# Performance work log

Hardware: AMD Instinct MI355X
Metric: run time of the kernel (lower is better)

Reference implementation:

```python
import jax, jax.numpy as jnp
import numpy as np

INPUT_SIZE = 1
HIDDEN = 30
B, T = 8192, 512


def setup_inputs() -> dict:
    key = jax.random.key(0)
    ks = jax.random.split(key, 7)
    s_ih = 1.0 / np.sqrt(HIDDEN)
    batch = jax.random.normal(ks[0], (B, T, INPUT_SIZE), dtype=jnp.float32)
    # PyTorch LSTM params: gate order i, f, g, o stacked along first dim (4H)
    W_ih = jax.random.uniform(ks[1], (4 * HIDDEN, INPUT_SIZE), minval=-s_ih, maxval=s_ih, dtype=jnp.float32)
    W_hh = jax.random.uniform(ks[2], (4 * HIDDEN, HIDDEN), minval=-s_ih, maxval=s_ih, dtype=jnp.float32)
    b_ih = jax.random.uniform(ks[3], (4 * HIDDEN,), minval=-s_ih, maxval=s_ih, dtype=jnp.float32)
    b_hh = jax.random.uniform(ks[4], (4 * HIDDEN,), minval=-s_ih, maxval=s_ih, dtype=jnp.float32)
    W_fc = jax.random.uniform(ks[5], (1, HIDDEN), minval=-s_ih, maxval=s_ih, dtype=jnp.float32)
    b_fc = jax.random.uniform(ks[6], (1,), minval=-s_ih, maxval=s_ih, dtype=jnp.float32)
    return {"batch": batch, "W_ih": W_ih, "W_hh": W_hh, "b_ih": b_ih, "b_hh": b_hh, "W_fc": W_fc, "b_fc": b_fc}


def _lstm_final_h(x, W_ih, W_hh, b_ih, b_hh):
    # x: [B, T, I] -> final hidden state h_T: [B, H]
    Bx = x.shape[0]
    H = W_hh.shape[1]
    # Precompute input-side gate projections for all timesteps: [T, B, 4H]
    xg = jnp.einsum('bti,gi->tbg', x, W_ih) + (b_ih + b_hh)

    def step(carry, xt):
        h, c = carry
        gates = xt + h @ W_hh.T  # [B, 4H]
        i, f, g, o = jnp.split(gates, 4, axis=-1)
        i = jax.nn.sigmoid(i)
        f = jax.nn.sigmoid(f)
        g = jnp.tanh(g)
        o = jax.nn.sigmoid(o)
        c = f * c + i * g
        h = o * jnp.tanh(c)
        return (h, c), None

    h0 = jnp.zeros((Bx, H), dtype=x.dtype)
    c0 = jnp.zeros((Bx, H), dtype=x.dtype)
    (hT, _), _ = jax.lax.scan(step, (h0, c0), xg)
    return hT


def reference(batch, W_ih, W_hh, b_ih, b_hh, W_fc, b_fc):
    hT = _lstm_final_h(batch, W_ih, W_hh, b_ih, b_hh)  # [B, H]
    out = hT @ W_fc.T + b_fc  # [B, 1]
    return out.squeeze(-1)  # [B]
```

## Files before the change

### kernel.cpp

```cpp
#include <hip/hip_runtime.h>

#define HID 30
#define TS  512
#define NB  16
#define LOG2E 1.44269504088896340736f
#define XSTR 17
#define HS   40

typedef __attribute__((ext_vector_type(8))) short bf16x8;
typedef __attribute__((ext_vector_type(4))) float f32x4;

__device__ __forceinline__ float rcp_f(float x){ return __builtin_amdgcn_rcpf(x); }
__device__ __forceinline__ float ex2_f(float x){ return __builtin_amdgcn_exp2f(x); }

__global__ __launch_bounds__(512, 4)
void lstm_mfma_u1(const float* __restrict__ batch,
                  const float* __restrict__ W_ih,
                  const float* __restrict__ W_hh,
                  const float* __restrict__ b_ih,
                  const float* __restrict__ b_hh,
                  const float* __restrict__ W_fc,
                  const float* __restrict__ b_fc,
                  float* __restrict__ out)
{
    __shared__ int xs[TS * XSTR];
    __shared__ __align__(16) short hhi[2][NB][HS];
    __shared__ __align__(16) short hlo[2][NB][HS];

    const int tid  = threadIdx.x;
    const int w    = tid >> 6;
    const int lane = tid & 63;
    const int q    = lane >> 4;
    const int col  = lane & 15;
    const int b0   = blockIdx.x * NB;

    #pragma unroll 4
    for (int i = 0; i < NB; ++i) {
        const float v = batch[(size_t)(b0 + i) * TS + tid];
        const __bf16 xh = (__bf16)v;
        const __bf16 xl = (__bf16)(v - (float)xh);
        xs[tid * XSTR + i] =
            (int)((unsigned)__builtin_bit_cast(unsigned short, xh) |
                 ((unsigned)__builtin_bit_cast(unsigned short, xl) << 16));
    }
    for (int i = tid; i < 2 * NB * HS / 2; i += 512) {
        ((int*)hhi)[i] = 0;
        ((int*)hlo)[i] = 0;
    }

    bf16x8 ahi, alo;
    {
        const int gate = col & 3;
        const int unit = 4 * w + (col >> 2);
        const float sG = (gate == 2) ? (-2.0f * LOG2E) : (-LOG2E);
        const int R = gate * HID + unit;
        #pragma unroll
        for (int jj = 0; jj < 8; ++jj) {
            const int kk = q * 8 + jj;
            float wv = 0.0f;
            if (unit < HID) {
                if (kk < HID)      wv = W_hh[R * HID + kk];
                else if (kk == 30) wv = b_ih[R] + b_hh[R];
                else               wv = W_ih[R];
            }
            wv *= sG;
            const __bf16 hi = (__bf16)wv;
            const __bf16 lo = (__bf16)(wv - (float)hi);
            ahi[jj] = (short)__builtin_bit_cast(unsigned short, hi);
            alo[jj] = (short)__builtin_bit_cast(unsigned short, lo);
        }
    }

    __syncthreads();

    const float TWOL = 2.0f * LOG2E;
    float cm = 0.0f;

#define STEP(T, RB, WB)                                                        \
{                                                                              \
    int4 vhi = *(const int4*)&hhi[RB][col][8 * q];                             \
    int4 vlo = *(const int4*)&hlo[RB][col][8 * q];                             \
    const unsigned xp = (unsigned)xs[(T) * XSTR + col];                        \
    vhi.w = (q == 3) ? (int)(0x3F80u | (xp << 16)) : vhi.w;                    \
    vlo.w = (q == 3) ? (int)(xp & 0xFFFF0000u)     : vlo.w;                    \
    const bf16x8 bhi = __builtin_bit_cast(bf16x8, vhi);                        \
    const bf16x8 blo = __builtin_bit_cast(bf16x8, vlo);                        \
    f32x4 a = {0.f, 0.f, 0.f, 0.f};                                            \
    a = __builtin_amdgcn_mfma_f32_16x16x32_bf16(ahi, bhi, a, 0, 0, 0);         \
    a = __builtin_amdgcn_mfma_f32_16x16x32_bf16(ahi, blo, a, 0, 0, 0);         \
    a = __builtin_amdgcn_mfma_f32_16x16x32_bf16(alo, bhi, a, 0, 0, 0);         \
                             \
    const float ei = ex2_f(a[0]), ef = ex2_f(a[1]);                            \
    const float eg = ex2_f(a[2]), eo = ex2_f(a[3]);                            \
    const float P  = (1.0f + ei) * (1.0f + eg);                                \
    const float Q  = 1.0f + ef;                                                \
    const float m1 = (eg - 1.0f) * Q;                                          \
    const float num = fmaf(TWOL, m1, cm * P);                                  \
    cm = num * rcp_f(P * Q);                                                   \
    const float e = ex2_f(cm);                                                 \
    const float h = (1.0f - e) * rcp_f((1.0f + e) * (1.0f + eo));              \
    const __bf16 hh = (__bf16)h;                                               \
    const __bf16 hl = (__bf16)(h - (float)hh);                                 \
    hhi[WB][col][4 * w + q] = (short)__builtin_bit_cast(unsigned short, hh);   \
    hlo[WB][col][4 * w + q] = (short)__builtin_bit_cast(unsigned short, hl);   \
    __syncthreads();                                                           \
}

    for (int t2 = 0; t2 < TS / 2; ++t2) {
        STEP(2 * t2,     0, 1)
        STEP(2 * t2 + 1, 1, 0)
    }
#undef STEP

    if (tid < NB) {
        const short* hh = &hhi[0][tid][0];
        const short* hl = &hlo[0][tid][0];
        float acc = b_fc[0];
        #pragma unroll
        for (int u = 0; u < HID; ++u) {
            const float hv =
                (float)__builtin_bit_cast(__bf16, (unsigned short)hh[u]) +
                (float)__builtin_bit_cast(__bf16, (unsigned short)hl[u]);
            acc = fmaf(hv, W_fc[u], acc);
        }
        out[b0 + tid] = acc;
    }
}

extern "C" void kernel_launch(void* const* d_in, const int* in_sizes, int n_in,
                              void* d_out, int out_size, void* d_ws, size_t ws_size,
                              hipStream_t stream) {
    const float* batch = (const float*)d_in[0];
    const float* W_ih  = (const float*)d_in[1];
    const float* W_hh  = (const float*)d_in[2];
    const float* b_ih  = (const float*)d_in[3];
    const float* b_hh  = (const float*)d_in[4];
    const float* W_fc  = (const float*)d_in[5];
    const float* b_fc  = (const float*)d_in[6];
    float* out = (float*)d_out;

    const int blocks = 8192 / NB;
    lstm_mfma_u1<<<blocks, 512, 0, stream>>>(batch, W_ih, W_hh, b_ih, b_hh,
                                             W_fc, b_fc, out);
}
```

Measured before the change: 186.9 us.

## Reorganize LDS hidden-state layout by k-group and split MFMA dependency chain

Changes the shared-memory hidden-state buffers from [buf][batch][40] to [buf][kgroup][batch][8], so each quad's 16-byte B-operand read is contiguous across columns. This is meant to cut LDS bank conflicts on both the reads and the scattered 2-byte writes. It also splits the three chained MFMAs into two independent accumulators summed at the end, shortening the serial MFMA latency on the recurrent critical path. The cost is four extra adds per step and a slightly different rounding order.

```diff
diff --git a/kernel.cpp b/kernel.cpp
--- a/kernel.cpp
+++ b/kernel.cpp
@@ -5,7 +5,6 @@
 #define NB  16
 #define LOG2E 1.44269504088896340736f
 #define XSTR 17
-#define HS   40
 
 typedef __attribute__((ext_vector_type(8))) short bf16x8;
 typedef __attribute__((ext_vector_type(4))) float f32x4;
@@ -14,18 +13,18 @@
 __device__ __forceinline__ float ex2_f(float x){ return __builtin_amdgcn_exp2f(x); }
 
 __global__ __launch_bounds__(512, 4)
-void lstm_mfma_u1(const float* __restrict__ batch,
-                  const float* __restrict__ W_ih,
-                  const float* __restrict__ W_hh,
-                  const float* __restrict__ b_ih,
-                  const float* __restrict__ b_hh,
-                  const float* __restrict__ W_fc,
-                  const float* __restrict__ b_fc,
-                  float* __restrict__ out)
+void lstm_mfma_u1e(const float* __restrict__ batch,
+                   const float* __restrict__ W_ih,
+                   const float* __restrict__ W_hh,
+                   const float* __restrict__ b_ih,
+                   const float* __restrict__ b_hh,
+                   const float* __restrict__ W_fc,
+                   const float* __restrict__ b_fc,
+                   float* __restrict__ out)
 {
     __shared__ int xs[TS * XSTR];
-    __shared__ __align__(16) short hhi[2][NB][HS];
-    __shared__ __align__(16) short hlo[2][NB][HS];
+    __shared__ __align__(16) short hhi[2][4][NB][8];
+    __shared__ __align__(16) short hlo[2][4][NB][8];
 
     const int tid  = threadIdx.x;
     const int w    = tid >> 6;
@@ -33,6 +32,9 @@
     const int q    = lane >> 4;
     const int col  = lane & 15;
     const int b0   = blockIdx.x * NB;
+    const int u4   = 4 * w + q;
+    const int g    = u4 >> 3;
+    const int s    = u4 & 7;
 
     #pragma unroll 4
     for (int i = 0; i < NB; ++i) {
@@ -43,7 +45,7 @@
             (int)((unsigned)__builtin_bit_cast(unsigned short, xh) |
                  ((unsigned)__builtin_bit_cast(unsigned short, xl) << 16));
     }
-    for (int i = tid; i < 2 * NB * HS / 2; i += 512) {
+    for (int i = tid; i < 2 * 4 * NB * 8 / 2; i += 512) {
         ((int*)hhi)[i] = 0;
         ((int*)hlo)[i] = 0;
     }
@@ -78,20 +80,25 @@
 
 #define STEP(T, RB, WB)                                                        \
 {                                                                              \
-    int4 vhi = *(const int4*)&hhi[RB][col][8 * q];                             \
-    int4 vlo = *(const int4*)&hlo[RB][col][8 * q];                             \
+    int4 vhi = *(const int4*)&hhi[RB][q][col][0];                              \
+    int4 vlo = *(const int4*)&hlo[RB][q][col][0];                              \
+      \
     const unsigned xp = (unsigned)xs[(T) * XSTR + col];                        \
     vhi.w = (q == 3) ? (int)(0x3F80u | (xp << 16)) : vhi.w;                    \
     vlo.w = (q == 3) ? (int)(xp & 0xFFFF0000u)     : vlo.w;                    \
     const bf16x8 bhi = __builtin_bit_cast(bf16x8, vhi);                        \
     const bf16x8 blo = __builtin_bit_cast(bf16x8, vlo);                        \
-    f32x4 a = {0.f, 0.f, 0.f, 0.f};                                            \
-    a = __builtin_amdgcn_mfma_f32_16x16x32_bf16(ahi, bhi, a, 0, 0, 0);         \
-    a = __builtin_amdgcn_mfma_f32_16x16x32_bf16(ahi, blo, a, 0, 0, 0);         \
-    a = __builtin_amdgcn_mfma_f32_16x16x32_bf16(alo, bhi, a, 0, 0, 0);         \
-                             \
-    const float ei = ex2_f(a[0]), ef = ex2_f(a[1]);                            \
-    const float eg = ex2_f(a[2]), eo = ex2_f(a[3]);                            \
+    const f32x4 z = {0.f, 0.f, 0.f, 0.f};                                      \
+     \
+    f32x4 accP = __builtin_amdgcn_mfma_f32_16x16x32_bf16(alo, bhi, z, 0, 0, 0);\
+    f32x4 accQ = __builtin_amdgcn_mfma_f32_16x16x32_bf16(ahi, blo, z, 0, 0, 0);\
+    accP = __builtin_amdgcn_mfma_f32_16x16x32_bf16(ahi, bhi, accP, 0, 0, 0);   \
+    const float ai = accP[0] + accQ[0];                                        \
+    const float af = accP[1] + accQ[1];                                        \
+    const float ag = accP[2] + accQ[2];                                        \
+    const float ao = accP[3] + accQ[3];                                        \
+    const float ei = ex2_f(ai), ef = ex2_f(af);                                \
+    const float eg = ex2_f(ag), eo = ex2_f(ao);                                \
     const float P  = (1.0f + ei) * (1.0f + eg);                                \
     const float Q  = 1.0f + ef;                                                \
     const float m1 = (eg - 1.0f) * Q;                                          \
@@ -101,8 +108,10 @@
     const float h = (1.0f - e) * rcp_f((1.0f + e) * (1.0f + eo));              \
     const __bf16 hh = (__bf16)h;                                               \
     const __bf16 hl = (__bf16)(h - (float)hh);                                 \
-    hhi[WB][col][4 * w + q] = (short)__builtin_bit_cast(unsigned short, hh);   \
-    hlo[WB][col][4 * w + q] = (short)__builtin_bit_cast(unsigned short, hl);   \
+     \
+     \
+    hhi[WB][g][col][s] = (short)__builtin_bit_cast(unsigned short, hh);        \
+    hlo[WB][g][col][s] = (short)__builtin_bit_cast(unsigned short, hl);        \
     __syncthreads();                                                           \
 }
 
@@ -113,14 +122,12 @@
 #undef STEP
 
     if (tid < NB) {
-        const short* hh = &hhi[0][tid][0];
-        const short* hl = &hlo[0][tid][0];
         float acc = b_fc[0];
         #pragma unroll
         for (int u = 0; u < HID; ++u) {
             const float hv =
-                (float)__builtin_bit_cast(__bf16, (unsigned short)hh[u]) +
-                (float)__builtin_bit_cast(__bf16, (unsigned short)hl[u]);
+                (float)__builtin_bit_cast(__bf16, (unsigned short)hhi[0][u >> 3][tid][u & 7]) +
+                (float)__builtin_bit_cast(__bf16, (unsigned short)hlo[0][u >> 3][tid][u & 7]);
             acc = fmaf(hv, W_fc[u], acc);
         }
         out[b0 + tid] = acc;
@@ -140,6 +147,6 @@
     float* out = (float*)d_out;
 
     const int blocks = 8192 / NB;
-    lstm_mfma_u1<<<blocks, 512, 0, stream>>>(batch, W_ih, W_hh, b_ih, b_hh,
-                                             W_fc, b_fc, out);
+    lstm_mfma_u1e<<<blocks, 512, 0, stream>>>(batch, W_ih, W_hh, b_ih, b_hh,
+                                              W_fc, b_fc, out);
 }
```

New measurement: 219.3 us. 1.17x slower.
